# Performance work log

Measured on AMD Instinct MI355X. Metric: run time of the kernel, lower is better.

Reference implementation:

```python
import jax, jax.numpy as jnp
import numpy as np

B, D, H, W_ = 2, 256, 64, 64


def setup_inputs() -> dict:
    key = jax.random.key(0)
    k1, k2 = jax.random.split(key)
    x = jax.random.normal(k1, (B, D, H, W_), dtype=jnp.float32)
    W = jax.random.normal(k2, (3 * D, D), dtype=jnp.float32) * 0.02  # 1x1 conv weight [out,in]
    b = jnp.zeros((3 * D,), dtype=jnp.float32)
    return {"x": x, "W": W, "b": b}


def reference(x, W, b):
    Bs, d, h, w = x.shape
    N = h * w
    sqrtV = d ** 0.25  # sqrt(sqrt(d)); q,k each divided -> qk^T / sqrt(d)
    # 1x1 conv == per-pixel linear over channels
    qkv = jnp.einsum('bchw,oc->bohw', x, W) + b[None, :, None, None]
    q, k, v = jnp.split(qkv, 3, axis=1)
    q = q.reshape(Bs, d, N).transpose(0, 2, 1) / sqrtV  # [B,N,d]
    k = k.reshape(Bs, d, N).transpose(0, 2, 1) / sqrtV
    v = v.reshape(Bs, d, N).transpose(0, 2, 1)
    # Sinkhorn (eps=1, max_iter=1, uniform marginals 1/N), log domain.
    # cost C = -q k^T  =>  -C = q k^T (softmax-style logits)
    negC = jnp.einsum('bnd,bmd->bnm', q, k)  # [B,N,N]
    logm = jnp.log(1.0 / N + 1e-8).astype(x.dtype)
    u = logm - jax.nn.logsumexp(negC, axis=-1)            # [B,N] row update
    vpot = logm - jax.nn.logsumexp(negC + u[..., None], axis=-2)  # [B,N] col update
    pi = jnp.exp(negC + u[..., None] + vpot[:, None, :])  # transport plan = attn
    out = jnp.einsum('bnm,bmd->bnd', pi, v)               # [B,N,d]
    return out.transpose(0, 2, 1).reshape(Bs, d, h, w)
```

## Files before the change

kernel.cpp:

```cpp
#include <hip/hip_runtime.h>
#include <hip/hip_bf16.h>
#include <math.h>

typedef __bf16 bf16;
typedef __bf16 bf16x8 __attribute__((ext_vector_type(8)));
typedef __bf16 bf16x4 __attribute__((ext_vector_type(4)));
typedef float floatx4 __attribute__((ext_vector_type(4)));

typedef const __attribute__((address_space(1))) void* gas_t;
typedef __attribute__((address_space(3))) void* las_t;

#define NPIX 4096
#define DCH 256

#define OFF_XB   ((size_t)0)
#define OFF_WB   ((size_t)4194304)
#define OFF_Q    ((size_t)4587520)
#define OFF_K    ((size_t)8781824)
#define OFF_V    ((size_t)12976128)
#define OFF_E    ((size_t)17170432)
#define OFF_VPP  ((size_t)84279296)
#define OFF_RP   ((size_t)88473600)
#define OFF_CP   ((size_t)89522176)
#define OFF_PART ((size_t)90570752)

__device__ __forceinline__ void stage_tile(const bf16* __restrict__ g0, size_t rstride,
                                           bf16* lds, int t) {
  const int wbase = (t >> 6) << 6;
#pragma unroll
  for (int i = 0; i < 4; i++) {
    int slot = i * 256 + t;
    int row = slot >> 3, seg = slot & 7;
    const bf16* g = g0 + (size_t)row * rstride + ((seg ^ (row & 7)) << 3);
    bf16* l = lds + (size_t)(i * 256 + wbase) * 8;
    __builtin_amdgcn_global_load_lds((gas_t)g, (las_t)l, 16, 0, 0);
  }
}


__global__ __launch_bounds__(256) void prep(
    const float* __restrict__ x, const float* __restrict__ W,
    bf16* __restrict__ xb, bf16* __restrict__ wb)
{
  const int t = threadIdx.x;
  if (blockIdx.y == 4) {
    int gid = (blockIdx.z * 64 + blockIdx.x) * 256 + t;
    for (int i = gid; i < 49152; i += 32768) {
      float4 v = *(const float4*)(W + (size_t)i * 4);
      bf16x4 pk = { (bf16)v.x, (bf16)v.y, (bf16)v.z, (bf16)v.w };
      *(bf16x4*)(wb + (size_t)i * 4) = pk;
    }
    return;
  }
  __shared__ float ts[64][65];
  const int b = blockIdx.z, n0 = blockIdx.x * 64, c0 = blockIdx.y * 64;
  const float* xp = x + ((size_t)b * DCH + c0) * NPIX + n0;
  for (int i = 0; i < 4; i++) {
    int slot = t + i * 256;
    int c = slot >> 4, nq = (slot & 15) * 4;
    float4 v = *(const float4*)(xp + (size_t)c * NPIX + nq);
    ts[c][nq + 0] = v.x; ts[c][nq + 1] = v.y; ts[c][nq + 2] = v.z; ts[c][nq + 3] = v.w;
  }
  __syncthreads();
  for (int i = 0; i < 2; i++) {
    int slot = t + i * 256;
    int n = slot >> 3, cq = (slot & 7) * 8;
    bf16x8 pk;
    for (int j = 0; j < 8; j++) pk[j] = (bf16)ts[cq + j][n];
    *(bf16x8*)(xb + ((size_t)b * NPIX + n0 + n) * DCH + c0 + cq) = pk;
  }
}

__global__ __launch_bounds__(256) void conv_mfma(
    const bf16* __restrict__ xb, const bf16* __restrict__ wb,
    const float* __restrict__ bias,
    bf16* __restrict__ qb, bf16* __restrict__ kb, bf16* __restrict__ vb)
{
  __shared__ bf16 at[2][128 * 64];
  __shared__ bf16 bt[2][128 * 64];
  __shared__ float bs[128];
  const int t  = threadIdx.x;
  const int n0 = blockIdx.x * 128;
  const int o0 = blockIdx.y * 128;
  if (t < 128) bs[t] = bias[o0 + t];
  const int lane = t & 63, wave = t >> 6;
  const int wm = wave >> 1, wn = wave & 1;
  const int l15 = lane & 15, quad = lane >> 4;
  const int l7 = l15 & 7;

  stage_tile(wb + (size_t)o0 * DCH, DCH, at[0], t);
  stage_tile(xb + (size_t)n0 * DCH, DCH, bt[0], t);

  floatx4 acc[4][4];
  for (int i=0;i<4;i++) for (int j=0;j<4;j++) for (int r=0;r<4;r++) acc[i][j][r] = 0.f;

#pragma unroll
  for (int kidx = 0; kidx < 4; kidx++) {
    const int cur = kidx & 1;
    if (kidx < 3) {
      stage_tile(wb + (size_t)o0 * DCH + (kidx + 1) * 64, DCH, at[cur ^ 1], t);
      stage_tile(xb + (size_t)n0 * DCH + (kidx + 1) * 64, DCH, bt[cur ^ 1], t);
      asm volatile("s_waitcnt vmcnt(8)" ::: "memory");
    } else {
      asm volatile("s_waitcnt vmcnt(0)" ::: "memory");
    }
    __builtin_amdgcn_s_barrier();
    asm volatile("" ::: "memory");
    for (int kk = 0; kk < 2; kk++) {
      bf16x8 af[4], bfr[4];
      int sw = ((kk * 4 + quad) ^ l7) * 8;
      for (int f = 0; f < 4; f++)
        af[f]  = *(const bf16x8*)&at[cur][(wm*64 + f*16 + l15)*64 + sw];
      for (int f = 0; f < 4; f++)
        bfr[f] = *(const bf16x8*)&bt[cur][(wn*64 + f*16 + l15)*64 + sw];
      for (int fm = 0; fm < 4; fm++)
        for (int fn = 0; fn < 4; fn++)
          acc[fm][fn] = __builtin_amdgcn_mfma_f32_16x16x32_bf16(af[fm], bfr[fn], acc[fm][fn], 0, 0, 0);
    }
    asm volatile("" ::: "memory");
    __builtin_amdgcn_s_barrier();
  }

  const float scale = (o0 < 512) ? 0.25f : 1.0f;
  bf16* dst; int od;
  if (o0 < 256)      { dst = qb; od = o0; }
  else if (o0 < 512) { dst = kb; od = o0 - 256; }
  else               { dst = vb; od = o0 - 512; }

  for (int fm = 0; fm < 4; fm++)
    for (int fn = 0; fn < 4; fn++) {
      int o_l = wm*64 + fm*16 + quad*4;
      int n_g = n0 + wn*64 + fn*16 + l15;
      bf16x4 pk;
      for (int r = 0; r < 4; r++)
        pk[r] = (bf16)((acc[fm][fn][r] + bs[o_l + r]) * scale);
      *(bf16x4*)(dst + (size_t)n_g * DCH + od + o_l) = pk;
    }
}

__global__ __launch_bounds__(256) void pass_a(
    const bf16* __restrict__ qb, const bf16* __restrict__ kb,
    bf16* __restrict__ E, float* __restrict__ rowpartG)
{
  __shared__ bf16 kt[2][128 * 64];
  __shared__ bf16 qt[2][128 * 64];
  __shared__ float rowpart[128];
  const int b = blockIdx.z;
  qb += (size_t)b * NPIX * DCH;
  kb += (size_t)b * NPIX * DCH;
  E  += (size_t)b * NPIX * NPIX;
  float* rp = rowpartG + ((size_t)b * 32 + blockIdx.x) * NPIX;
  const int t  = threadIdx.x;
  const int m0 = blockIdx.x * 128;
  const int n0 = blockIdx.y * 128;
  const int lane = t & 63, wave = t >> 6;
  const int wm = wave >> 1, wn = wave & 1;
  const int l15 = lane & 15, quad = lane >> 4;
  const int l7 = l15 & 7;

  stage_tile(kb + (size_t)m0 * DCH, DCH, kt[0], t);
  stage_tile(qb + (size_t)n0 * DCH, DCH, qt[0], t);

  floatx4 acc[4][4];
  for (int i=0;i<4;i++) for (int j=0;j<4;j++) for (int r=0;r<4;r++) acc[i][j][r] = 0.f;

#pragma unroll
  for (int kidx = 0; kidx < 4; kidx++) {
    const int cur = kidx & 1;
    if (kidx < 3) {
      stage_tile(kb + (size_t)m0 * DCH + (kidx + 1) * 64, DCH, kt[cur ^ 1], t);
      stage_tile(qb + (size_t)n0 * DCH + (kidx + 1) * 64, DCH, qt[cur ^ 1], t);
      asm volatile("s_waitcnt vmcnt(8)" ::: "memory");
    } else {
      asm volatile("s_waitcnt vmcnt(0)" ::: "memory");
    }
    __builtin_amdgcn_s_barrier();
    asm volatile("" ::: "memory");
    for (int kk = 0; kk < 2; kk++) {
      bf16x8 af[4], bfr[4];
      int sw = ((kk * 4 + quad) ^ l7) * 8;
      for (int f = 0; f < 4; f++)
        af[f]  = *(const bf16x8*)&kt[cur][(wm*64 + f*16 + l15)*64 + sw];
      for (int f = 0; f < 4; f++)
        bfr[f] = *(const bf16x8*)&qt[cur][(wn*64 + f*16 + l15)*64 + sw];
      for (int fm = 0; fm < 4; fm++)
        for (int fn = 0; fn < 4; fn++)
          acc[fm][fn] = __builtin_amdgcn_mfma_f32_16x16x32_bf16(af[fm], bfr[fn], acc[fm][fn], 0, 0, 0);
    }
    asm volatile("" ::: "memory");
    __builtin_amdgcn_s_barrier();
  }

  if (t < 128) rowpart[t] = 0.f;
  __syncthreads();

  float rsum[4] = {0.f, 0.f, 0.f, 0.f};
  for (int fm = 0; fm < 4; fm++)
    for (int fn = 0; fn < 4; fn++) {
      int n_g = n0 + wn*64 + fn*16 + l15;
      int m_g = m0 + wm*64 + fm*16 + quad*4;
      bf16x4 pk;
      float s = 0.f;
      for (int r = 0; r < 4; r++) {
        float e = __expf(acc[fm][fn][r]);
        pk[r] = (bf16)e;
        s += e;
      }
      *(bf16x4*)(E + (size_t)n_g * NPIX + m_g) = pk;
      rsum[fn] += s;
    }
  for (int fn = 0; fn < 4; fn++) {
    float s = rsum[fn];
    s += __shfl_xor(s, 16);
    s += __shfl_xor(s, 32);
    if (quad == 0) atomicAdd(&rowpart[wn*64 + fn*16 + l15], s);
  }
  __syncthreads();
  if (t < 128) rp[n0 + t] = rowpart[t];
}

__global__ __launch_bounds__(256) void col_pass(
    const bf16* __restrict__ E, const float* __restrict__ rowpartG,
    float* __restrict__ colpartG, float logm)
{
  __shared__ float eus[128];
  const int b = blockIdx.z;
  E += (size_t)b * NPIX * NPIX;
  const float* rp = rowpartG + (size_t)b * 32 * NPIX;
  float* cp = colpartG + ((size_t)b * 32 + blockIdx.y) * NPIX;
  const int t = threadIdx.x;
  const int col = blockIdx.x * 1024 + t * 4;
  const int nbase = blockIdx.y * 128;
  if (t < 128) {
    float s = 0.f;
    for (int mi = 0; mi < 32; mi++) s += rp[(size_t)mi * NPIX + nbase + t];
    eus[t] = __expf(logm - __logf(s));
  }
  __syncthreads();
  float a0 = 0.f, a1 = 0.f, a2 = 0.f, a3 = 0.f;
  for (int r = 0; r < 128; r++) {
    float eu = eus[r];
    bf16x4 ev = *(const bf16x4*)(E + (size_t)(nbase + r) * NPIX + col);
    a0 += eu * (float)ev[0];
    a1 += eu * (float)ev[1];
    a2 += eu * (float)ev[2];
    a3 += eu * (float)ev[3];
  }
  float4 o = {a0, a1, a2, a3};
  *(float4*)(cp + col) = o;
}

__global__ __launch_bounds__(256) void vpp_kernel(
    const bf16* __restrict__ vb, const float* __restrict__ colpartG,
    bf16* __restrict__ vppT, float logm)
{
  __shared__ float ts[64][65];
  __shared__ float ef[64];
  const int b = blockIdx.z;
  vb += (size_t)b * NPIX * DCH;
  const float* cp = colpartG + (size_t)b * 32 * NPIX;
  vppT += (size_t)b * DCH * NPIX;
  const int t = threadIdx.x;
  const int m0 = blockIdx.x * 64, d0 = blockIdx.y * 64;
  if (t < 64) {
    float s = 0.f;
    for (int g = 0; g < 32; g++) s += cp[(size_t)g * NPIX + m0 + t];
    ef[t] = __expf(logm - __logf(s));
  }
  __syncthreads();
  for (int i = 0; i < 2; i++) {
    int slot = t + i * 256;
    int m = slot >> 3, dq = (slot & 7) * 8;
    bf16x8 v = *(const bf16x8*)(vb + (size_t)(m0 + m) * DCH + d0 + dq);
    float s = ef[m];
    for (int j = 0; j < 8; j++) ts[dq + j][m] = s * (float)v[j];
  }
  __syncthreads();
  for (int i = 0; i < 2; i++) {
    int slot = t + i * 256;
    int d = slot >> 3, mq = (slot & 7) * 8;
    bf16x8 pk;
    for (int j = 0; j < 8; j++) pk[j] = (bf16)ts[d][mq + j];
    *(bf16x8*)(vppT + (size_t)(d0 + d) * NPIX + m0 + mq) = pk;
  }
}

__global__ __launch_bounds__(256) void pass_c(
    const bf16* __restrict__ E, const bf16* __restrict__ vppT,
    const float* __restrict__ rowpartG, bf16* __restrict__ part, float logm)
{
  __shared__ bf16 et[2][128 * 64];
  __shared__ bf16 vt[2][128 * 64];
  __shared__ float eus[128];
  const int z = blockIdx.z;
  const int b = z >> 2, kc = z & 3;
  E += (size_t)b * NPIX * NPIX;
  vppT += (size_t)b * DCH * NPIX;
  const float* rp = rowpartG + (size_t)b * 32 * NPIX;
  part += (size_t)(b * 4 + kc) * DCH * NPIX;
  const int t  = threadIdx.x;
  const int n0 = blockIdx.x * 128;
  const int d0 = blockIdx.y * 128;
  const int mstart = kc * 1024;
  if (t < 128) {
    float s = 0.f;
    for (int mi = 0; mi < 32; mi++) s += rp[(size_t)mi * NPIX + n0 + t];
    eus[t] = __expf(logm - __logf(s));
  }
  const int lane = t & 63, wave = t >> 6;
  const int wn = wave >> 1, wd = wave & 1;
  const int l15 = lane & 15, quad = lane >> 4;
  const int l7 = l15 & 7;

  floatx4 acc[4][4];
  for (int i=0;i<4;i++) for (int j=0;j<4;j++) for (int r=0;r<4;r++) acc[i][j][r] = 0.f;
  __syncthreads();

  stage_tile(E + (size_t)n0 * NPIX + mstart, NPIX, et[0], t);
  stage_tile(vppT + (size_t)d0 * NPIX + mstart, NPIX, vt[0], t);

#pragma unroll 4
  for (int kidx = 0; kidx < 16; kidx++) {
    const int cur = kidx & 1;
    if (kidx < 15) {
      const int kn = mstart + (kidx + 1) * 64;
      stage_tile(E + (size_t)n0 * NPIX + kn, NPIX, et[cur ^ 1], t);
      stage_tile(vppT + (size_t)d0 * NPIX + kn, NPIX, vt[cur ^ 1], t);
      asm volatile("s_waitcnt vmcnt(8)" ::: "memory");
    } else {
      asm volatile("s_waitcnt vmcnt(0)" ::: "memory");
    }
    __builtin_amdgcn_s_barrier();
    asm volatile("" ::: "memory");
    for (int kk = 0; kk < 2; kk++) {
      bf16x8 af[4], bfr[4];
      int sw = ((kk * 4 + quad) ^ l7) * 8;
      for (int f = 0; f < 4; f++)
        af[f]  = *(const bf16x8*)&et[cur][(wn*64 + f*16 + l15)*64 + sw];
      for (int f = 0; f < 4; f++)
        bfr[f] = *(const bf16x8*)&vt[cur][(wd*64 + f*16 + l15)*64 + sw];
      for (int fn = 0; fn < 4; fn++)
        for (int fd = 0; fd < 4; fd++)
          acc[fn][fd] = __builtin_amdgcn_mfma_f32_16x16x32_bf16(af[fn], bfr[fd], acc[fn][fd], 0, 0, 0);
    }
    asm volatile("" ::: "memory");
    __builtin_amdgcn_s_barrier();
  }

  for (int fn = 0; fn < 4; fn++)
    for (int fd = 0; fd < 4; fd++) {
      int d_g = d0 + wd*64 + fd*16 + l15;
      int n_l = wn*64 + fn*16 + quad*4;
      bf16x4 o;
      o[0] = (bf16)(acc[fn][fd][0] * eus[n_l + 0]);
      o[1] = (bf16)(acc[fn][fd][1] * eus[n_l + 1]);
      o[2] = (bf16)(acc[fn][fd][2] * eus[n_l + 2]);
      o[3] = (bf16)(acc[fn][fd][3] * eus[n_l + 3]);
      *(bf16x4*)(part + (size_t)d_g * NPIX + n0 + n_l) = o;
    }
}

__global__ __launch_bounds__(256) void reduce_k(
    const bf16* __restrict__ part, float* __restrict__ outp)
{
  size_t i4 = ((size_t)blockIdx.x * 256 + threadIdx.x) * 4;
  size_t b = i4 >> 20;
  size_t off = i4 & (size_t)1048575;
  const bf16* p = part + b * 4 * (size_t)1048576 + off;
  bf16x4 a = *(const bf16x4*)(p);
  bf16x4 bq = *(const bf16x4*)(p + (size_t)1048576);
  bf16x4 c = *(const bf16x4*)(p + (size_t)2097152);
  bf16x4 d = *(const bf16x4*)(p + (size_t)3145728);
  float4 s = { (float)a[0]+(float)bq[0]+(float)c[0]+(float)d[0],
               (float)a[1]+(float)bq[1]+(float)c[1]+(float)d[1],
               (float)a[2]+(float)bq[2]+(float)c[2]+(float)d[2],
               (float)a[3]+(float)bq[3]+(float)c[3]+(float)d[3] };
  *(float4*)(outp + i4) = s;
}

extern "C" void kernel_launch(void* const* d_in, const int* in_sizes, int n_in,
                              void* d_out, int out_size, void* d_ws, size_t ws_size,
                              hipStream_t stream) {
  (void)in_sizes; (void)n_in; (void)out_size; (void)ws_size;
  const float* x    = (const float*)d_in[0];
  const float* Wm   = (const float*)d_in[1];
  const float* bias = (const float*)d_in[2];
  float* outp = (float*)d_out;
  char* ws = (char*)d_ws;

  bf16*  xb   = (bf16*)(ws + OFF_XB);
  bf16*  wb   = (bf16*)(ws + OFF_WB);
  bf16*  qb   = (bf16*)(ws + OFF_Q);
  bf16*  kb   = (bf16*)(ws + OFF_K);
  bf16*  vb   = (bf16*)(ws + OFF_V);
  bf16*  E    = (bf16*)(ws + OFF_E);
  bf16*  vppT = (bf16*)(ws + OFF_VPP);
  float* rp   = (float*)(ws + OFF_RP);
  float* cp   = (float*)(ws + OFF_CP);
  bf16*  part = (bf16*)(ws + OFF_PART);

  const float logm = logf(1.0f / 4096.0f + 1e-8f);

  prep<<<dim3(64, 5, 2), 256, 0, stream>>>(x, Wm, xb, wb);
  conv_mfma<<<dim3(64, 6), 256, 0, stream>>>(xb, wb, bias, qb, kb, vb);

  pass_a<<<dim3(32, 32, 2), 256, 0, stream>>>(qb, kb, E, rp);
  col_pass<<<dim3(4, 32, 2), 256, 0, stream>>>(E, rp, cp, logm);
  vpp_kernel<<<dim3(64, 4, 2), 256, 0, stream>>>(vb, cp, vppT, logm);
  pass_c<<<dim3(32, 2, 8), 256, 0, stream>>>(E, vppT, rp, part, logm);
  reduce_k<<<2048, 256, 0, stream>>>(part, outp);
}
```

Baseline: 157.3 us.

## Enlarge pass_a and pass_c tiles to 512 threads with LDS-staged coalesced stores

pass_a now computes 256x256 tiles of E per 512-thread block, with a block-index swizzle so neighbouring blocks share rows. Results go through LDS so E is written as full 16-byte rows, and row sums are taken from that same readback. This drops the shared-memory atomics and halves the row-partial buffer, which col_pass and pass_c now read with 16 partials instead of 32. pass_c covers all 256 d channels per block, so each E tile is loaded once instead of twice, and it also writes its output through an LDS transpose. The cost is larger LDS use, more registers (8x4 accumulators in pass_a), fewer blocks in the grid, and lower occupancy.

```diff
diff --git a/kernel.cpp b/kernel.cpp
--- a/kernel.cpp
+++ b/kernel.cpp
@@ -37,6 +37,31 @@
   }
 }
 
+__device__ __forceinline__ void stage_tile512(const bf16* __restrict__ g0, size_t rstride,
+                                              bf16* lds, int t) {
+  const int wbase = (t >> 6) << 6;
+#pragma unroll
+  for (int i = 0; i < 4; i++) {
+    int slot = i * 512 + t;
+    int row = slot >> 3, seg = slot & 7;
+    const bf16* g = g0 + (size_t)row * rstride + ((seg ^ (row & 7)) << 3);
+    bf16* l = lds + (size_t)(i * 512 + wbase) * 8;
+    __builtin_amdgcn_global_load_lds((gas_t)g, (las_t)l, 16, 0, 0);
+  }
+}
+
+__device__ __forceinline__ void stage_tile128_512(const bf16* __restrict__ g0, size_t rstride,
+                                                  bf16* lds, int t) {
+  const int wbase = (t >> 6) << 6;
+#pragma unroll
+  for (int i = 0; i < 2; i++) {
+    int slot = i * 512 + t;
+    int row = slot >> 3, seg = slot & 7;
+    const bf16* g = g0 + (size_t)row * rstride + ((seg ^ (row & 7)) << 3);
+    bf16* l = lds + (size_t)(i * 512 + wbase) * 8;
+    __builtin_amdgcn_global_load_lds((gas_t)g, (las_t)l, 16, 0, 0);
+  }
+}
 
 __global__ __launch_bounds__(256) void prep(
     const float* __restrict__ x, const float* __restrict__ W,
@@ -138,38 +163,40 @@
     }
 }
 
-__global__ __launch_bounds__(256) void pass_a(
+__global__ __launch_bounds__(512, 2) void pass_a(
     const bf16* __restrict__ qb, const bf16* __restrict__ kb,
     bf16* __restrict__ E, float* __restrict__ rowpartG)
 {
-  __shared__ bf16 kt[2][128 * 64];
-  __shared__ bf16 qt[2][128 * 64];
-  __shared__ float rowpart[128];
-  const int b = blockIdx.z;
+  __shared__ bf16 smem[65536];
+  int flat = (int)blockIdx.x + ((int)blockIdx.y << 4) + ((int)blockIdx.z << 8);
+  flat = (flat & 7) * 64 + (flat >> 3);
+  const int bx = flat & 15, by = (flat >> 4) & 15, b = flat >> 8;
   qb += (size_t)b * NPIX * DCH;
   kb += (size_t)b * NPIX * DCH;
   E  += (size_t)b * NPIX * NPIX;
-  float* rp = rowpartG + ((size_t)b * 32 + blockIdx.x) * NPIX;
+  float* rp = rowpartG + ((size_t)b * 16 + bx) * NPIX;
   const int t  = threadIdx.x;
-  const int m0 = blockIdx.x * 128;
-  const int n0 = blockIdx.y * 128;
+  const int m0 = bx * 256;
+  const int n0 = by * 256;
   const int lane = t & 63, wave = t >> 6;
-  const int wm = wave >> 1, wn = wave & 1;
+  const int wm = wave >> 2, wn = wave & 3;
   const int l15 = lane & 15, quad = lane >> 4;
   const int l7 = l15 & 7;
-
-  stage_tile(kb + (size_t)m0 * DCH, DCH, kt[0], t);
-  stage_tile(qb + (size_t)n0 * DCH, DCH, qt[0], t);
-
-  floatx4 acc[4][4];
-  for (int i=0;i<4;i++) for (int j=0;j<4;j++) for (int r=0;r<4;r++) acc[i][j][r] = 0.f;
+  bf16* kt0 = smem;
+  bf16* qt0 = smem + 32768;
+
+  stage_tile512(kb + (size_t)m0 * DCH, DCH, kt0, t);
+  stage_tile512(qb + (size_t)n0 * DCH, DCH, qt0, t);
+
+  floatx4 acc[8][4];
+  for (int i=0;i<8;i++) for (int j=0;j<4;j++) for (int r=0;r<4;r++) acc[i][j][r] = 0.f;
 
 #pragma unroll
   for (int kidx = 0; kidx < 4; kidx++) {
     const int cur = kidx & 1;
     if (kidx < 3) {
-      stage_tile(kb + (size_t)m0 * DCH + (kidx + 1) * 64, DCH, kt[cur ^ 1], t);
-      stage_tile(qb + (size_t)n0 * DCH + (kidx + 1) * 64, DCH, qt[cur ^ 1], t);
+      stage_tile512(kb + (size_t)m0 * DCH + (kidx + 1) * 64, DCH, kt0 + (cur ^ 1) * 16384, t);
+      stage_tile512(qb + (size_t)n0 * DCH + (kidx + 1) * 64, DCH, qt0 + (cur ^ 1) * 16384, t);
       asm volatile("s_waitcnt vmcnt(8)" ::: "memory");
     } else {
       asm volatile("s_waitcnt vmcnt(0)" ::: "memory");
@@ -177,13 +204,13 @@
     __builtin_amdgcn_s_barrier();
     asm volatile("" ::: "memory");
     for (int kk = 0; kk < 2; kk++) {
-      bf16x8 af[4], bfr[4];
+      bf16x8 af[8], bfr[4];
       int sw = ((kk * 4 + quad) ^ l7) * 8;
+      for (int f = 0; f < 8; f++)
+        af[f]  = *(const bf16x8*)&kt0[cur*16384 + (wm*128 + f*16 + l15)*64 + sw];
       for (int f = 0; f < 4; f++)
-        af[f]  = *(const bf16x8*)&kt[cur][(wm*64 + f*16 + l15)*64 + sw];
-      for (int f = 0; f < 4; f++)
-        bfr[f] = *(const bf16x8*)&qt[cur][(wn*64 + f*16 + l15)*64 + sw];
-      for (int fm = 0; fm < 4; fm++)
+        bfr[f] = *(const bf16x8*)&qt0[cur*16384 + (wn*64 + f*16 + l15)*64 + sw];
+      for (int fm = 0; fm < 8; fm++)
         for (int fn = 0; fn < 4; fn++)
           acc[fm][fn] = __builtin_amdgcn_mfma_f32_16x16x32_bf16(af[fm], bfr[fn], acc[fm][fn], 0, 0, 0);
     }
@@ -191,32 +218,32 @@
     __builtin_amdgcn_s_barrier();
   }
 
-  if (t < 128) rowpart[t] = 0.f;
-  __syncthreads();
-
-  float rsum[4] = {0.f, 0.f, 0.f, 0.f};
-  for (int fm = 0; fm < 4; fm++)
+  bf16* ep = smem;
+  for (int fm = 0; fm < 8; fm++)
     for (int fn = 0; fn < 4; fn++) {
-      int n_g = n0 + wn*64 + fn*16 + l15;
-      int m_g = m0 + wm*64 + fm*16 + quad*4;
+      int n_loc = wn*64 + fn*16 + l15;
+      int mby  = (wm*128 + fm*16 + quad*4) * 2;
+      int addr = n_loc * 512 + mby;
+      addr ^= (n_loc & 7) << 4;
       bf16x4 pk;
-      float s = 0.f;
-      for (int r = 0; r < 4; r++) {
-        float e = __expf(acc[fm][fn][r]);
-        pk[r] = (bf16)e;
-        s += e;
-      }
-      *(bf16x4*)(E + (size_t)n_g * NPIX + m_g) = pk;
-      rsum[fn] += s;
-    }
-  for (int fn = 0; fn < 4; fn++) {
-    float s = rsum[fn];
-    s += __shfl_xor(s, 16);
-    s += __shfl_xor(s, 32);
-    if (quad == 0) atomicAdd(&rowpart[wn*64 + fn*16 + l15], s);
-  }
-  __syncthreads();
-  if (t < 128) rp[n0 + t] = rowpart[t];
+      for (int r = 0; r < 4; r++) pk[r] = (bf16)__expf(acc[fm][fn][r]);
+      *(bf16x4*)((char*)ep + addr) = pk;
+    }
+  __syncthreads();
+#pragma unroll
+  for (int i = 0; i < 16; i++) {
+    int slot = i * 512 + t;
+    int nr = slot >> 5, c = slot & 31;
+    int addr = nr * 512 + c * 16;
+    addr ^= (nr & 7) << 4;
+    bf16x8 v = *(const bf16x8*)((char*)ep + addr);
+    *(bf16x8*)(E + (size_t)(n0 + nr) * NPIX + m0 + c * 8) = v;
+    float s = 0.f;
+    for (int j = 0; j < 8; j++) s += (float)v[j];
+    s += __shfl_xor(s, 1); s += __shfl_xor(s, 2); s += __shfl_xor(s, 4);
+    s += __shfl_xor(s, 8); s += __shfl_xor(s, 16);
+    if ((t & 31) == 0) rp[n0 + nr] = s;
+  }
 }
 
 __global__ __launch_bounds__(256) void col_pass(
@@ -226,14 +253,14 @@
   __shared__ float eus[128];
   const int b = blockIdx.z;
   E += (size_t)b * NPIX * NPIX;
-  const float* rp = rowpartG + (size_t)b * 32 * NPIX;
+  const float* rp = rowpartG + (size_t)b * 16 * NPIX;
   float* cp = colpartG + ((size_t)b * 32 + blockIdx.y) * NPIX;
   const int t = threadIdx.x;
   const int col = blockIdx.x * 1024 + t * 4;
   const int nbase = blockIdx.y * 128;
   if (t < 128) {
     float s = 0.f;
-    for (int mi = 0; mi < 32; mi++) s += rp[(size_t)mi * NPIX + nbase + t];
+    for (int mi = 0; mi < 16; mi++) s += rp[(size_t)mi * NPIX + nbase + t];
     eus[t] = __expf(logm - __logf(s));
   }
   __syncthreads();
@@ -285,48 +312,48 @@
   }
 }
 
-__global__ __launch_bounds__(256) void pass_c(
+__global__ __launch_bounds__(512, 2) void pass_c(
     const bf16* __restrict__ E, const bf16* __restrict__ vppT,
     const float* __restrict__ rowpartG, bf16* __restrict__ part, float logm)
 {
-  __shared__ bf16 et[2][128 * 64];
-  __shared__ bf16 vt[2][128 * 64];
+  __shared__ bf16 smem[49152];
   __shared__ float eus[128];
   const int z = blockIdx.z;
   const int b = z >> 2, kc = z & 3;
   E += (size_t)b * NPIX * NPIX;
   vppT += (size_t)b * DCH * NPIX;
-  const float* rp = rowpartG + (size_t)b * 32 * NPIX;
+  const float* rpg = rowpartG + (size_t)b * 16 * NPIX;
   part += (size_t)(b * 4 + kc) * DCH * NPIX;
   const int t  = threadIdx.x;
   const int n0 = blockIdx.x * 128;
-  const int d0 = blockIdx.y * 128;
   const int mstart = kc * 1024;
   if (t < 128) {
     float s = 0.f;
-    for (int mi = 0; mi < 32; mi++) s += rp[(size_t)mi * NPIX + n0 + t];
+    for (int mi = 0; mi < 16; mi++) s += rpg[(size_t)mi * NPIX + n0 + t];
     eus[t] = __expf(logm - __logf(s));
   }
   const int lane = t & 63, wave = t >> 6;
-  const int wn = wave >> 1, wd = wave & 1;
+  const int wn = wave >> 2, wd = wave & 3;
   const int l15 = lane & 15, quad = lane >> 4;
   const int l7 = l15 & 7;
+  bf16* et0 = smem;
+  bf16* vt0 = smem + 16384;
 
   floatx4 acc[4][4];
   for (int i=0;i<4;i++) for (int j=0;j<4;j++) for (int r=0;r<4;r++) acc[i][j][r] = 0.f;
   __syncthreads();
 
-  stage_tile(E + (size_t)n0 * NPIX + mstart, NPIX, et[0], t);
-  stage_tile(vppT + (size_t)d0 * NPIX + mstart, NPIX, vt[0], t);
+  stage_tile128_512(E + (size_t)n0 * NPIX + mstart, NPIX, et0, t);
+  stage_tile512(vppT + mstart, NPIX, vt0, t);
 
 #pragma unroll 4
   for (int kidx = 0; kidx < 16; kidx++) {
     const int cur = kidx & 1;
     if (kidx < 15) {
       const int kn = mstart + (kidx + 1) * 64;
-      stage_tile(E + (size_t)n0 * NPIX + kn, NPIX, et[cur ^ 1], t);
-      stage_tile(vppT + (size_t)d0 * NPIX + kn, NPIX, vt[cur ^ 1], t);
-      asm volatile("s_waitcnt vmcnt(8)" ::: "memory");
+      stage_tile128_512(E + (size_t)n0 * NPIX + kn, NPIX, et0 + (cur ^ 1) * 8192, t);
+      stage_tile512(vppT + kn, NPIX, vt0 + (cur ^ 1) * 16384, t);
+      asm volatile("s_waitcnt vmcnt(6)" ::: "memory");
     } else {
       asm volatile("s_waitcnt vmcnt(0)" ::: "memory");
     }
@@ -336,9 +363,9 @@
       bf16x8 af[4], bfr[4];
       int sw = ((kk * 4 + quad) ^ l7) * 8;
       for (int f = 0; f < 4; f++)
-        af[f]  = *(const bf16x8*)&et[cur][(wn*64 + f*16 + l15)*64 + sw];
+        af[f]  = *(const bf16x8*)&et0[cur*8192  + (wn*64 + f*16 + l15)*64 + sw];
       for (int f = 0; f < 4; f++)
-        bfr[f] = *(const bf16x8*)&vt[cur][(wd*64 + f*16 + l15)*64 + sw];
+        bfr[f] = *(const bf16x8*)&vt0[cur*16384 + (wd*64 + f*16 + l15)*64 + sw];
       for (int fn = 0; fn < 4; fn++)
         for (int fd = 0; fd < 4; fd++)
           acc[fn][fd] = __builtin_amdgcn_mfma_f32_16x16x32_bf16(af[fn], bfr[fd], acc[fn][fd], 0, 0, 0);
@@ -347,17 +374,27 @@
     __builtin_amdgcn_s_barrier();
   }
 
+  bf16* ept = smem;
   for (int fn = 0; fn < 4; fn++)
     for (int fd = 0; fd < 4; fd++) {
-      int d_g = d0 + wd*64 + fd*16 + l15;
-      int n_l = wn*64 + fn*16 + quad*4;
+      int d_loc = wd*64 + fd*16 + l15;
+      int n_l   = wn*64 + fn*16 + quad*4;
+      int addr = d_loc * 256 + n_l * 2;
+      addr ^= (d_loc & 7) << 4;
       bf16x4 o;
-      o[0] = (bf16)(acc[fn][fd][0] * eus[n_l + 0]);
-      o[1] = (bf16)(acc[fn][fd][1] * eus[n_l + 1]);
-      o[2] = (bf16)(acc[fn][fd][2] * eus[n_l + 2]);
-      o[3] = (bf16)(acc[fn][fd][3] * eus[n_l + 3]);
-      *(bf16x4*)(part + (size_t)d_g * NPIX + n0 + n_l) = o;
-    }
+      for (int r = 0; r < 4; r++) o[r] = (bf16)(acc[fn][fd][r] * eus[n_l + r]);
+      *(bf16x4*)((char*)ept + addr) = o;
+    }
+  __syncthreads();
+#pragma unroll
+  for (int i = 0; i < 8; i++) {
+    int slot = i * 512 + t;
+    int dr = slot >> 4, c = slot & 15;
+    int addr = dr * 256 + c * 16;
+    addr ^= (dr & 7) << 4;
+    bf16x8 v = *(const bf16x8*)((char*)ept + addr);
+    *(bf16x8*)(part + (size_t)dr * NPIX + n0 + c * 8) = v;
+  }
 }
 
 __global__ __launch_bounds__(256) void reduce_k(
@@ -404,9 +441,9 @@
   prep<<<dim3(64, 5, 2), 256, 0, stream>>>(x, Wm, xb, wb);
   conv_mfma<<<dim3(64, 6), 256, 0, stream>>>(xb, wb, bias, qb, kb, vb);
 
-  pass_a<<<dim3(32, 32, 2), 256, 0, stream>>>(qb, kb, E, rp);
+  pass_a<<<dim3(16, 16, 2), 512, 0, stream>>>(qb, kb, E, rp);
   col_pass<<<dim3(4, 32, 2), 256, 0, stream>>>(E, rp, cp, logm);
   vpp_kernel<<<dim3(64, 4, 2), 256, 0, stream>>>(vb, cp, vppT, logm);
-  pass_c<<<dim3(32, 2, 8), 256, 0, stream>>>(E, vppT, rp, part, logm);
+  pass_c<<<dim3(32, 1, 8), 512, 0, stream>>>(E, vppT, rp, part, logm);
   reduce_k<<<2048, 256, 0, stream>>>(part, outp);
 }
```

Result: faster. 152.6 us (-3.0%).
